# Performance work log

Hardware: AMD Instinct MI355X
Metric: run time of the kernel (lower is better)

Reference implementation:

```python
import jax, jax.numpy as jnp
import numpy as np

POSE_DIM = 16
H_DIM = 32
SEQ_LEN = 25
BATCH = 262144


def setup_inputs() -> dict:
    key = jax.random.key(0)
    ks = jax.random.split(key, 9)
    s = 0.1  # keep gates out of saturation
    return {
        "first_input": jax.random.normal(ks[0], (BATCH, POSE_DIM), dtype=jnp.float32),
        "h0": jax.random.normal(ks[1], (BATCH, H_DIM), dtype=jnp.float32),
        "c0": jax.random.normal(ks[2], (BATCH, H_DIM), dtype=jnp.float32),
        # LSTM params, torch layout/gate order (i, f, g, o)
        "W_ih": s * jax.random.normal(ks[3], (4 * H_DIM, POSE_DIM), dtype=jnp.float32),
        "W_hh": s * jax.random.normal(ks[4], (4 * H_DIM, H_DIM), dtype=jnp.float32),
        "b_ih": s * jax.random.normal(ks[5], (4 * H_DIM,), dtype=jnp.float32),
        "b_hh": s * jax.random.normal(ks[6], (4 * H_DIM,), dtype=jnp.float32),
        # hidden -> input-space projection
        "W_out": s * jax.random.normal(ks[7], (POSE_DIM, H_DIM), dtype=jnp.float32),
        "b_out": s * jax.random.normal(ks[8], (POSE_DIM,), dtype=jnp.float32),
    }


def reference(first_input, h0, c0, W_ih, W_hh, b_ih, b_hh, W_out, b_out):
    # Gate order matches torch.nn.LSTM: i, f, g, o.
    b = b_ih + b_hh  # [4H]

    def step(carry, _):
        x, h, c = carry  # x: [B, P], h/c: [B, H]
        gates = x @ W_ih.T + h @ W_hh.T + b  # [B, 4H]
        i, f, g, o = jnp.split(gates, 4, axis=-1)
        c = jax.nn.sigmoid(f) * c + jax.nn.sigmoid(i) * jnp.tanh(g)
        h = jax.nn.sigmoid(o) * jnp.tanh(c)
        x_next = h @ W_out.T + b_out  # projected back to pose space [B, P]
        return (x_next, h, c), x_next

    _, preds = jax.lax.scan(step, (first_input, h0, c0), None, length=SEQ_LEN)
    # preds: [S, B, P] -> [B, S, P] to match torch cat along dim=1
    return jnp.transpose(preds, (1, 0, 2))
```

## Files before the change

### kernel.cpp

```cpp
#include <hip/hip_runtime.h>
#include <hip/hip_bf16.h>


constexpr int P = 16;
constexpr int H = 32;
constexpr int S = 25;

typedef short        bf16x8 __attribute__((ext_vector_type(8)));
typedef float        f32x16 __attribute__((ext_vector_type(16)));
typedef float        f32x4  __attribute__((ext_vector_type(4)));
typedef unsigned int u32x4  __attribute__((ext_vector_type(4)));

union FragU { u32x4 u; bf16x8 b; };

#if __has_builtin(__builtin_amdgcn_exp2f)
#define EX2 __builtin_amdgcn_exp2f
#else
#define EX2 exp2f
#endif

__device__ __forceinline__ unsigned int pkbf(float lo, float hi) {
    unsigned short a = __builtin_bit_cast(unsigned short, __float2bfloat16(lo));
    unsigned short b = __builtin_bit_cast(unsigned short, __float2bfloat16(hi));
    return (unsigned int)a | ((unsigned int)b << 16);
}

__device__ __forceinline__ float gate_scale(int r) {
    return (r >= 64 && r < 96) ? -2.8853900817779268f
                               : -1.4426950408889634f;
}

__global__ void setup_frags(const float* __restrict__ Wih, const float* __restrict__ Whh,
                            const float* __restrict__ bih, const float* __restrict__ bhh,
                            const float* __restrict__ Wout, const float* __restrict__ bout,
                            unsigned int* __restrict__ ws)
{
    auto waug = [&](int r, int k) -> float {
        float s = (r < 128) ? gate_scale(r) : 1.0f;
        if (r < 128) {
            if (k < 32) {
                float a = Whh[r * H + k];
                for (int p = 0; p < P; ++p) a += Wih[r * P + p] * Wout[p * H + k];
                return s * a;
            }
            if (k == 32) {
                float a = bih[r] + bhh[r];
                for (int p = 0; p < P; ++p) a += Wih[r * P + p] * bout[p];
                return s * a;
            }
            return 0.0f;
        } else if (r < 144) {
            int p = r - 128;
            if (k < 32)  return Wout[p * H + k];
            if (k == 32) return bout[p];
            return 0.0f;
        }
        return 0.0f;
    };
    auto w0aug = [&](int r, int k) -> float {
        float s = gate_scale(r);
        if (k < 16)  return s * Wih[r * P + k];
        if (k < 48)  return s * Whh[r * H + (k - 16)];
        if (k == 48) return s * (bih[r] + bhh[r]);
        return 0.0f;
    };

    const int tid = threadIdx.x;
    for (int idx = tid; idx < 5 * 3 * 64 * 4; idx += 256) {
        int v = idx & 3, l = (idx >> 2) & 63, tc = idx >> 8;
        int t = tc / 3, c = tc % 3;
        int r = 32 * t + (l & 31);
        int k = 16 * c + 8 * (v >> 1) + 4 * (l >> 5) + 2 * (v & 1);
        ws[idx] = pkbf(waug(r, k), waug(r, k + 1));
    }
    for (int idx = tid; idx < 4 * 4 * 64 * 4; idx += 256) {
        int v = idx & 3, l = (idx >> 2) & 63, tc = idx >> 8;
        int t = tc / 4, c = tc % 4;
        int r = 32 * t + (l & 31);
        int k = 16 * c + 8 * (v >> 1) + 4 * (l >> 5) + 2 * (v & 1);
        ws[3840 + idx] = pkbf(w0aug(r, k), w0aug(r, k + 1));
    }
}

__global__ __launch_bounds__(256, 2) void decoder_mfma(
    const float* __restrict__ x0, const float* __restrict__ h0,
    const float* __restrict__ c0, const unsigned int* __restrict__ ws,
    float* __restrict__ out, int batch)
{
    const int lane = threadIdx.x & 63;
    const int wid  = threadIdx.x >> 6;
    const int bcol = lane & 31;
    const int hi   = lane >> 5;
    const int bg   = (blockIdx.x * 4 + wid) * 32 + bcol;
    if (bg >= batch) return;

    FragU A[5][3];
    #pragma unroll
    for (int t = 0; t < 5; ++t)
        #pragma unroll
        for (int c = 0; c < 3; ++c)
            A[t][c].u = *reinterpret_cast<const u32x4*>(ws + ((t * 3 + c) * 64 + lane) * 4);

    FragU Bbias;
    Bbias.u.x = (hi == 0) ? 0x3F80u : 0u;
    Bbias.u.y = 0u; Bbias.u.z = 0u; Bbias.u.w = 0u;

    float cc[16];
    #pragma unroll
    for (int q = 0; q < 4; ++q) {
        f32x4 t = *reinterpret_cast<const f32x4*>(c0 + (size_t)bg * H + q * 8 + 4 * hi);
        cc[q * 4 + 0] = t.x; cc[q * 4 + 1] = t.y; cc[q * 4 + 2] = t.z; cc[q * 4 + 3] = t.w;
    }

    const f32x16 vzero = {};
    f32x16 acc[4];

    {
        FragU B0[4];
        {
            const float* p = x0 + (size_t)bg * P;
            f32x4 a  = *reinterpret_cast<const f32x4*>(p + 4 * hi);
            f32x4 b4 = *reinterpret_cast<const f32x4*>(p + 8 + 4 * hi);
            B0[0].u.x = pkbf(a.x, a.y);  B0[0].u.y = pkbf(a.z, a.w);
            B0[0].u.z = pkbf(b4.x, b4.y); B0[0].u.w = pkbf(b4.z, b4.w);
        }
        #pragma unroll
        for (int ch = 0; ch < 2; ++ch) {
            const float* p = h0 + (size_t)bg * H + 16 * ch;
            f32x4 a  = *reinterpret_cast<const f32x4*>(p + 4 * hi);
            f32x4 b4 = *reinterpret_cast<const f32x4*>(p + 8 + 4 * hi);
            B0[1 + ch].u.x = pkbf(a.x, a.y);  B0[1 + ch].u.y = pkbf(a.z, a.w);
            B0[1 + ch].u.z = pkbf(b4.x, b4.y); B0[1 + ch].u.w = pkbf(b4.z, b4.w);
        }
        B0[3] = Bbias;

        #pragma unroll
        for (int t = 0; t < 4; ++t) acc[t] = vzero;
        #pragma unroll
        for (int c4 = 0; c4 < 4; ++c4) {
            #pragma unroll
            for (int t = 0; t < 4; ++t) {
                FragU a;
                a.u = *reinterpret_cast<const u32x4*>(ws + 3840 + ((t * 4 + c4) * 64 + lane) * 4);
                acc[t] = __builtin_amdgcn_mfma_f32_32x32x16_bf16(a.b, B0[c4].b, acc[t], 0, 0, 0);
            }
        }
    }

    FragU Bh[2];
    for (int s = 0; s < S; ++s) {
        float hh[16];
        #pragma unroll
        for (int r = 0; r < 16; ++r) {
            const float ei = EX2(acc[0][r]);
            const float ef = EX2(acc[1][r]);
            const float eg = EX2(acc[2][r]);
            const float eo = EX2(acc[3][r]);
            const float r1 = __builtin_amdgcn_rcpf((1.0f + ei) * (1.0f + eg));
            const float tg = (1.0f - eg) * r1;
            const float rf = __builtin_amdgcn_rcpf(1.0f + ef);
            const float cn = __builtin_fmaf(cc[r], rf, tg);
            cc[r] = cn;
            const float ec = EX2(cn * -2.8853900817779268f);
            const float r2 = __builtin_amdgcn_rcpf((1.0f + ec) * (1.0f + eo));
            hh[r] = (1.0f - ec) * r2;
        }

        Bh[0].u.x = pkbf(hh[0],  hh[1]);  Bh[0].u.y = pkbf(hh[2],  hh[3]);
        Bh[0].u.z = pkbf(hh[4],  hh[5]);  Bh[0].u.w = pkbf(hh[6],  hh[7]);
        Bh[1].u.x = pkbf(hh[8],  hh[9]);  Bh[1].u.y = pkbf(hh[10], hh[11]);
        Bh[1].u.z = pkbf(hh[12], hh[13]); Bh[1].u.w = pkbf(hh[14], hh[15]);

        f32x16 px;
        px = __builtin_amdgcn_mfma_f32_32x32x16_bf16(A[4][2].b, Bbias.b, vzero, 0, 0, 0);
        px = __builtin_amdgcn_mfma_f32_32x32x16_bf16(A[4][0].b, Bh[0].b, px,    0, 0, 0);
        px = __builtin_amdgcn_mfma_f32_32x32x16_bf16(A[4][1].b, Bh[1].b, px,    0, 0, 0);

        float* op = out + ((size_t)bg * S + s) * P + 4 * hi;
        f32x4 v0; v0.x = px[0]; v0.y = px[1]; v0.z = px[2]; v0.w = px[3];
        f32x4 v1; v1.x = px[4]; v1.y = px[5]; v1.z = px[6]; v1.w = px[7];
        __builtin_nontemporal_store(v0, reinterpret_cast<f32x4*>(op));
        __builtin_nontemporal_store(v1, reinterpret_cast<f32x4*>(op + 8));

        if (s + 1 < S) {
            #pragma unroll
            for (int t = 0; t < 4; ++t)
                acc[t] = __builtin_amdgcn_mfma_f32_32x32x16_bf16(A[t][2].b, Bbias.b, vzero, 0, 0, 0);
            #pragma unroll
            for (int ch = 0; ch < 2; ++ch)
                #pragma unroll
                for (int t = 0; t < 4; ++t)
                    acc[t] = __builtin_amdgcn_mfma_f32_32x32x16_bf16(A[t][ch].b, Bh[ch].b, acc[t], 0, 0, 0);
        }
    }
}

extern "C" void kernel_launch(void* const* d_in, const int* in_sizes, int n_in,
                              void* d_out, int out_size, void* d_ws, size_t ws_size,
                              hipStream_t stream) {
    const float* x0   = (const float*)d_in[0];
    const float* h0   = (const float*)d_in[1];
    const float* c0   = (const float*)d_in[2];
    const float* Wih  = (const float*)d_in[3];
    const float* Whh  = (const float*)d_in[4];
    const float* bih  = (const float*)d_in[5];
    const float* bhh  = (const float*)d_in[6];
    const float* Wout = (const float*)d_in[7];
    const float* bout = (const float*)d_in[8];
    float* out = (float*)d_out;
    unsigned int* ws = (unsigned int*)d_ws;

    const int batch = in_sizes[0] / P;

    hipLaunchKernelGGL(setup_frags, dim3(1), dim3(256), 0, stream,
                       Wih, Whh, bih, bhh, Wout, bout, ws);

    dim3 block(256);
    dim3 grid((batch + 127) / 128);
    hipLaunchKernelGGL(decoder_mfma, grid, block, 0, stream,
                       x0, h0, c0, ws, out, batch);
}
```

Before: 228.4 us.

## Process two independent batch tiles per wave to overlap MFMA and elementwise work

```diff
diff --git a/kernel.cpp b/kernel.cpp
--- a/kernel.cpp
+++ b/kernel.cpp
@@ -9,6 +9,7 @@
 typedef short        bf16x8 __attribute__((ext_vector_type(8)));
 typedef float        f32x16 __attribute__((ext_vector_type(16)));
 typedef float        f32x4  __attribute__((ext_vector_type(4)));
+typedef float        f32x2  __attribute__((ext_vector_type(2)));
 typedef unsigned int u32x4  __attribute__((ext_vector_type(4)));
 
 union FragU { u32x4 u; bf16x8 b; };
@@ -91,8 +92,10 @@
     const int wid  = threadIdx.x >> 6;
     const int bcol = lane & 31;
     const int hi   = lane >> 5;
-    const int bg   = (blockIdx.x * 4 + wid) * 32 + bcol;
-    if (bg >= batch) return;
+    const int base = (blockIdx.x * 4 + wid) * 64;
+    const int bg0  = base + bcol;
+    const int bg1  = base + 32 + bcol;
+    if (bg1 >= batch) return;
 
     FragU A[5][3];
     #pragma unroll
@@ -105,93 +108,126 @@
     Bbias.u.x = (hi == 0) ? 0x3F80u : 0u;
     Bbias.u.y = 0u; Bbias.u.z = 0u; Bbias.u.w = 0u;
 
-    float cc[16];
+    f32x2 cc0[8], cc1[8];
     #pragma unroll
     for (int q = 0; q < 4; ++q) {
-        f32x4 t = *reinterpret_cast<const f32x4*>(c0 + (size_t)bg * H + q * 8 + 4 * hi);
-        cc[q * 4 + 0] = t.x; cc[q * 4 + 1] = t.y; cc[q * 4 + 2] = t.z; cc[q * 4 + 3] = t.w;
+        f32x4 t0 = *reinterpret_cast<const f32x4*>(c0 + (size_t)bg0 * H + q * 8 + 4 * hi);
+        cc0[2 * q]     = f32x2{t0.x, t0.y};
+        cc0[2 * q + 1] = f32x2{t0.z, t0.w};
+        f32x4 t1 = *reinterpret_cast<const f32x4*>(c0 + (size_t)bg1 * H + q * 8 + 4 * hi);
+        cc1[2 * q]     = f32x2{t1.x, t1.y};
+        cc1[2 * q + 1] = f32x2{t1.z, t1.w};
     }
 
     const f32x16 vzero = {};
-    f32x16 acc[4];
+    f32x16 acc0[4], acc1[4];
+
+    auto EW = [&](f32x16 (&acc)[4], f32x2 (&cc)[8], f32x2 (&hh)[8]) {
+        const f32x2 one = {1.0f, 1.0f};
+        const f32x2 nk2 = {-2.8853900817779268f, -2.8853900817779268f};
+        #pragma unroll
+        for (int i = 0; i < 8; ++i) {
+            f32x2 Fi = {acc[0][2 * i], acc[0][2 * i + 1]};
+            f32x2 Ff = {acc[1][2 * i], acc[1][2 * i + 1]};
+            f32x2 Fg = {acc[2][2 * i], acc[2][2 * i + 1]};
+            f32x2 Fo = {acc[3][2 * i], acc[3][2 * i + 1]};
+            f32x2 ei, ef, eg, eo;
+            ei.x = EX2(Fi.x); ei.y = EX2(Fi.y);
+            ef.x = EX2(Ff.x); ef.y = EX2(Ff.y);
+            eg.x = EX2(Fg.x); eg.y = EX2(Fg.y);
+            eo.x = EX2(Fo.x); eo.y = EX2(Fo.y);
+            f32x2 d1 = (one + ei) * (one + eg);
+            f32x2 r1; r1.x = __builtin_amdgcn_rcpf(d1.x); r1.y = __builtin_amdgcn_rcpf(d1.y);
+            f32x2 tg = (one - eg) * r1;
+            f32x2 df = one + ef;
+            f32x2 rf; rf.x = __builtin_amdgcn_rcpf(df.x); rf.y = __builtin_amdgcn_rcpf(df.y);
+            f32x2 cn = cc[i] * rf + tg;
+            cc[i] = cn;
+            f32x2 ar = cn * nk2;
+            f32x2 ec; ec.x = EX2(ar.x); ec.y = EX2(ar.y);
+            f32x2 d2 = (one + ec) * (one + eo);
+            f32x2 r2; r2.x = __builtin_amdgcn_rcpf(d2.x); r2.y = __builtin_amdgcn_rcpf(d2.y);
+            hh[i] = (one - ec) * r2;
+        }
+    };
+    auto PACK = [&](f32x2 (&hh)[8], FragU (&Bh)[2]) {
+        Bh[0].u.x = pkbf(hh[0].x, hh[0].y); Bh[0].u.y = pkbf(hh[1].x, hh[1].y);
+        Bh[0].u.z = pkbf(hh[2].x, hh[2].y); Bh[0].u.w = pkbf(hh[3].x, hh[3].y);
+        Bh[1].u.x = pkbf(hh[4].x, hh[4].y); Bh[1].u.y = pkbf(hh[5].x, hh[5].y);
+        Bh[1].u.z = pkbf(hh[6].x, hh[6].y); Bh[1].u.w = pkbf(hh[7].x, hh[7].y);
+    };
+    auto PROJSTORE = [&](FragU (&Bh)[2], int bg, int s) {
+        f32x16 px;
+        px = __builtin_amdgcn_mfma_f32_32x32x16_bf16(A[4][2].b, Bbias.b, vzero, 0, 0, 0);
+        px = __builtin_amdgcn_mfma_f32_32x32x16_bf16(A[4][0].b, Bh[0].b, px,    0, 0, 0);
+        px = __builtin_amdgcn_mfma_f32_32x32x16_bf16(A[4][1].b, Bh[1].b, px,    0, 0, 0);
+        float* op = out + ((size_t)bg * S + s) * P + 4 * hi;
+        f32x4 v0 = {px[0], px[1], px[2], px[3]};
+        f32x4 v1 = {px[4], px[5], px[6], px[7]};
+        __builtin_nontemporal_store(v0, reinterpret_cast<f32x4*>(op));
+        __builtin_nontemporal_store(v1, reinterpret_cast<f32x4*>(op + 8));
+    };
+    auto GATES = [&](f32x16 (&acc)[4], FragU (&Bh)[2]) {
+        #pragma unroll
+        for (int t = 0; t < 4; ++t) {
+            f32x16 a;
+            a = __builtin_amdgcn_mfma_f32_32x32x16_bf16(A[t][2].b, Bbias.b, vzero, 0, 0, 0);
+            a = __builtin_amdgcn_mfma_f32_32x32x16_bf16(A[t][0].b, Bh[0].b, a,    0, 0, 0);
+            a = __builtin_amdgcn_mfma_f32_32x32x16_bf16(A[t][1].b, Bh[1].b, a,    0, 0, 0);
+            acc[t] = a;
+        }
+    };
 
     {
-        FragU B0[4];
+        FragU B00[4], B01[4];
         {
-            const float* p = x0 + (size_t)bg * P;
+            const float* p = x0 + (size_t)bg0 * P;
             f32x4 a  = *reinterpret_cast<const f32x4*>(p + 4 * hi);
             f32x4 b4 = *reinterpret_cast<const f32x4*>(p + 8 + 4 * hi);
-            B0[0].u.x = pkbf(a.x, a.y);  B0[0].u.y = pkbf(a.z, a.w);
-            B0[0].u.z = pkbf(b4.x, b4.y); B0[0].u.w = pkbf(b4.z, b4.w);
+            B00[0].u.x = pkbf(a.x, a.y);   B00[0].u.y = pkbf(a.z, a.w);
+            B00[0].u.z = pkbf(b4.x, b4.y); B00[0].u.w = pkbf(b4.z, b4.w);
+            p = x0 + (size_t)bg1 * P;
+            a  = *reinterpret_cast<const f32x4*>(p + 4 * hi);
+            b4 = *reinterpret_cast<const f32x4*>(p + 8 + 4 * hi);
+            B01[0].u.x = pkbf(a.x, a.y);   B01[0].u.y = pkbf(a.z, a.w);
+            B01[0].u.z = pkbf(b4.x, b4.y); B01[0].u.w = pkbf(b4.z, b4.w);
         }
         #pragma unroll
         for (int ch = 0; ch < 2; ++ch) {
-            const float* p = h0 + (size_t)bg * H + 16 * ch;
-            f32x4 a  = *reinterpret_cast<const f32x4*>(p + 4 * hi);
-            f32x4 b4 = *reinterpret_cast<const f32x4*>(p + 8 + 4 * hi);
-            B0[1 + ch].u.x = pkbf(a.x, a.y);  B0[1 + ch].u.y = pkbf(a.z, a.w);
-            B0[1 + ch].u.z = pkbf(b4.x, b4.y); B0[1 + ch].u.w = pkbf(b4.z, b4.w);
-        }
-        B0[3] = Bbias;
-
-        #pragma unroll
-        for (int t = 0; t < 4; ++t) acc[t] = vzero;
-        #pragma unroll
-        for (int c4 = 0; c4 < 4; ++c4) {
+            const float* q = h0 + (size_t)bg0 * H + 16 * ch;
+            f32x4 c4 = *reinterpret_cast<const f32x4*>(q + 4 * hi);
+            f32x4 d4 = *reinterpret_cast<const f32x4*>(q + 8 + 4 * hi);
+            B00[1 + ch].u.x = pkbf(c4.x, c4.y); B00[1 + ch].u.y = pkbf(c4.z, c4.w);
+            B00[1 + ch].u.z = pkbf(d4.x, d4.y); B00[1 + ch].u.w = pkbf(d4.z, d4.w);
+            q = h0 + (size_t)bg1 * H + 16 * ch;
+            c4 = *reinterpret_cast<const f32x4*>(q + 4 * hi);
+            d4 = *reinterpret_cast<const f32x4*>(q + 8 + 4 * hi);
+            B01[1 + ch].u.x = pkbf(c4.x, c4.y); B01[1 + ch].u.y = pkbf(c4.z, c4.w);
+            B01[1 + ch].u.z = pkbf(d4.x, d4.y); B01[1 + ch].u.w = pkbf(d4.z, d4.w);
+        }
+        B00[3] = Bbias; B01[3] = Bbias;
+        #pragma unroll
+        for (int t = 0; t < 4; ++t) { acc0[t] = vzero; acc1[t] = vzero; }
+        #pragma unroll
+        for (int c4 = 0; c4 < 4; ++c4)
             #pragma unroll
             for (int t = 0; t < 4; ++t) {
                 FragU a;
                 a.u = *reinterpret_cast<const u32x4*>(ws + 3840 + ((t * 4 + c4) * 64 + lane) * 4);
-                acc[t] = __builtin_amdgcn_mfma_f32_32x32x16_bf16(a.b, B0[c4].b, acc[t], 0, 0, 0);
+                acc0[t] = __builtin_amdgcn_mfma_f32_32x32x16_bf16(a.b, B00[c4].b, acc0[t], 0, 0, 0);
+                acc1[t] = __builtin_amdgcn_mfma_f32_32x32x16_bf16(a.b, B01[c4].b, acc1[t], 0, 0, 0);
             }
-        }
-    }
-
-    FragU Bh[2];
+    }
+
     for (int s = 0; s < S; ++s) {
-        float hh[16];
-        #pragma unroll
-        for (int r = 0; r < 16; ++r) {
-            const float ei = EX2(acc[0][r]);
-            const float ef = EX2(acc[1][r]);
-            const float eg = EX2(acc[2][r]);
-            const float eo = EX2(acc[3][r]);
-            const float r1 = __builtin_amdgcn_rcpf((1.0f + ei) * (1.0f + eg));
-            const float tg = (1.0f - eg) * r1;
-            const float rf = __builtin_amdgcn_rcpf(1.0f + ef);
-            const float cn = __builtin_fmaf(cc[r], rf, tg);
-            cc[r] = cn;
-            const float ec = EX2(cn * -2.8853900817779268f);
-            const float r2 = __builtin_amdgcn_rcpf((1.0f + ec) * (1.0f + eo));
-            hh[r] = (1.0f - ec) * r2;
-        }
-
-        Bh[0].u.x = pkbf(hh[0],  hh[1]);  Bh[0].u.y = pkbf(hh[2],  hh[3]);
-        Bh[0].u.z = pkbf(hh[4],  hh[5]);  Bh[0].u.w = pkbf(hh[6],  hh[7]);
-        Bh[1].u.x = pkbf(hh[8],  hh[9]);  Bh[1].u.y = pkbf(hh[10], hh[11]);
-        Bh[1].u.z = pkbf(hh[12], hh[13]); Bh[1].u.w = pkbf(hh[14], hh[15]);
-
-        f32x16 px;
-        px = __builtin_amdgcn_mfma_f32_32x32x16_bf16(A[4][2].b, Bbias.b, vzero, 0, 0, 0);
-        px = __builtin_amdgcn_mfma_f32_32x32x16_bf16(A[4][0].b, Bh[0].b, px,    0, 0, 0);
-        px = __builtin_amdgcn_mfma_f32_32x32x16_bf16(A[4][1].b, Bh[1].b, px,    0, 0, 0);
-
-        float* op = out + ((size_t)bg * S + s) * P + 4 * hi;
-        f32x4 v0; v0.x = px[0]; v0.y = px[1]; v0.z = px[2]; v0.w = px[3];
-        f32x4 v1; v1.x = px[4]; v1.y = px[5]; v1.z = px[6]; v1.w = px[7];
-        __builtin_nontemporal_store(v0, reinterpret_cast<f32x4*>(op));
-        __builtin_nontemporal_store(v1, reinterpret_cast<f32x4*>(op + 8));
-
-        if (s + 1 < S) {
-            #pragma unroll
-            for (int t = 0; t < 4; ++t)
-                acc[t] = __builtin_amdgcn_mfma_f32_32x32x16_bf16(A[t][2].b, Bbias.b, vzero, 0, 0, 0);
-            #pragma unroll
-            for (int ch = 0; ch < 2; ++ch)
-                #pragma unroll
-                for (int t = 0; t < 4; ++t)
-                    acc[t] = __builtin_amdgcn_mfma_f32_32x32x16_bf16(A[t][ch].b, Bh[ch].b, acc[t], 0, 0, 0);
-        }
+        f32x2 hh0[8]; FragU Bh0[2];
+        EW(acc0, cc0, hh0); PACK(hh0, Bh0);
+        PROJSTORE(Bh0, bg0, s);
+        if (s + 1 < S) GATES(acc0, Bh0);
+        f32x2 hh1[8]; FragU Bh1[2];
+        EW(acc1, cc1, hh1); PACK(hh1, Bh1);
+        PROJSTORE(Bh1, bg1, s);
+        if (s + 1 < S) GATES(acc1, Bh1);
     }
 }
 
@@ -216,7 +252,7 @@
                        Wih, Whh, bih, bhh, Wout, bout, ws);
 
     dim3 block(256);
-    dim3 grid((batch + 127) / 128);
+    dim3 grid((batch + 255) / 256);
     hipLaunchKernelGGL(decoder_mfma, grid, block, 0, stream,
                        x0, h0, c0, ws, out, batch);
 }
```

New measurement: 224.9 us. No clear change (-1.6%).

## Stage weight fragments in LDS and raise occupancy to four blocks per CU

Applied to the files above, without the earlier changes.

```diff
diff --git a/kernel.cpp b/kernel.cpp
--- a/kernel.cpp
+++ b/kernel.cpp
@@ -82,24 +82,29 @@
     }
 }
 
-__global__ __launch_bounds__(256, 2) void decoder_mfma(
+__global__ __launch_bounds__(256, 4) void decoder_mfma(
     const float* __restrict__ x0, const float* __restrict__ h0,
     const float* __restrict__ c0, const unsigned int* __restrict__ ws,
     float* __restrict__ out, int batch)
 {
+    __shared__ unsigned int Alds[5 * 3 * 64 * 4];
+
     const int lane = threadIdx.x & 63;
     const int wid  = threadIdx.x >> 6;
     const int bcol = lane & 31;
     const int hi   = lane >> 5;
     const int bg   = (blockIdx.x * 4 + wid) * 32 + bcol;
+
+    for (int i = threadIdx.x; i < 5 * 3 * 64 * 4; i += 256) Alds[i] = ws[i];
+    __syncthreads();
     if (bg >= batch) return;
 
-    FragU A[5][3];
-    #pragma unroll
-    for (int t = 0; t < 5; ++t)
-        #pragma unroll
-        for (int c = 0; c < 3; ++c)
-            A[t][c].u = *reinterpret_cast<const u32x4*>(ws + ((t * 3 + c) * 64 + lane) * 4);
+    const unsigned int* const Abase = Alds + lane * 4;
+    auto ldA = [&](int t, int c) -> FragU {
+        FragU a;
+        a.u = *reinterpret_cast<const u32x4*>(Abase + (t * 3 + c) * 256);
+        return a;
+    };
 
     FragU Bbias;
     Bbias.u.x = (hi == 0) ? 0x3F80u : 0u;
@@ -114,6 +119,7 @@
 
     const f32x16 vzero = {};
     f32x16 acc[4];
+    FragU Bh[2];
 
     {
         FragU B0[4];
@@ -147,51 +153,57 @@
         }
     }
 
-    FragU Bh[2];
-    for (int s = 0; s < S; ++s) {
-        float hh[16];
-        #pragma unroll
-        for (int r = 0; r < 16; ++r) {
-            const float ei = EX2(acc[0][r]);
-            const float ef = EX2(acc[1][r]);
-            const float eg = EX2(acc[2][r]);
-            const float eo = EX2(acc[3][r]);
-            const float r1 = __builtin_amdgcn_rcpf((1.0f + ei) * (1.0f + eg));
-            const float tg = (1.0f - eg) * r1;
-            const float rf = __builtin_amdgcn_rcpf(1.0f + ef);
-            const float cn = __builtin_fmaf(cc[r], rf, tg);
-            cc[r] = cn;
-            const float ec = EX2(cn * -2.8853900817779268f);
-            const float r2 = __builtin_amdgcn_rcpf((1.0f + ec) * (1.0f + eo));
-            hh[r] = (1.0f - ec) * r2;
-        }
-
-        Bh[0].u.x = pkbf(hh[0],  hh[1]);  Bh[0].u.y = pkbf(hh[2],  hh[3]);
-        Bh[0].u.z = pkbf(hh[4],  hh[5]);  Bh[0].u.w = pkbf(hh[6],  hh[7]);
-        Bh[1].u.x = pkbf(hh[8],  hh[9]);  Bh[1].u.y = pkbf(hh[10], hh[11]);
-        Bh[1].u.z = pkbf(hh[12], hh[13]); Bh[1].u.w = pkbf(hh[14], hh[15]);
-
+    auto EWPACK = [&]() {
+        #pragma unroll
+        for (int i = 0; i < 8; ++i) {
+            float h2[2];
+            #pragma unroll
+            for (int j = 0; j < 2; ++j) {
+                const int r = 2 * i + j;
+                const float ei = EX2(acc[0][r]);
+                const float ef = EX2(acc[1][r]);
+                const float eg = EX2(acc[2][r]);
+                const float eo = EX2(acc[3][r]);
+                const float r1 = __builtin_amdgcn_rcpf((1.0f + ei) * (1.0f + eg));
+                const float tg = (1.0f - eg) * r1;
+                const float rf = __builtin_amdgcn_rcpf(1.0f + ef);
+                const float cn = __builtin_fmaf(cc[r], rf, tg);
+                cc[r] = cn;
+                const float ec = EX2(cn * -2.8853900817779268f);
+                const float r2 = __builtin_amdgcn_rcpf((1.0f + ec) * (1.0f + eo));
+                h2[j] = (1.0f - ec) * r2;
+            }
+            Bh[i >> 2].u[i & 3] = pkbf(h2[0], h2[1]);
+        }
+    };
+    auto PROJSTORE = [&](int s) {
+        FragU a;
         f32x16 px;
-        px = __builtin_amdgcn_mfma_f32_32x32x16_bf16(A[4][2].b, Bbias.b, vzero, 0, 0, 0);
-        px = __builtin_amdgcn_mfma_f32_32x32x16_bf16(A[4][0].b, Bh[0].b, px,    0, 0, 0);
-        px = __builtin_amdgcn_mfma_f32_32x32x16_bf16(A[4][1].b, Bh[1].b, px,    0, 0, 0);
-
+        a = ldA(4, 2); px = __builtin_amdgcn_mfma_f32_32x32x16_bf16(a.b, Bbias.b, vzero, 0, 0, 0);
+        a = ldA(4, 0); px = __builtin_amdgcn_mfma_f32_32x32x16_bf16(a.b, Bh[0].b, px,    0, 0, 0);
+        a = ldA(4, 1); px = __builtin_amdgcn_mfma_f32_32x32x16_bf16(a.b, Bh[1].b, px,    0, 0, 0);
         float* op = out + ((size_t)bg * S + s) * P + 4 * hi;
-        f32x4 v0; v0.x = px[0]; v0.y = px[1]; v0.z = px[2]; v0.w = px[3];
-        f32x4 v1; v1.x = px[4]; v1.y = px[5]; v1.z = px[6]; v1.w = px[7];
+        f32x4 v0 = {px[0], px[1], px[2], px[3]};
+        f32x4 v1 = {px[4], px[5], px[6], px[7]};
         __builtin_nontemporal_store(v0, reinterpret_cast<f32x4*>(op));
         __builtin_nontemporal_store(v1, reinterpret_cast<f32x4*>(op + 8));
-
-        if (s + 1 < S) {
-            #pragma unroll
-            for (int t = 0; t < 4; ++t)
-                acc[t] = __builtin_amdgcn_mfma_f32_32x32x16_bf16(A[t][2].b, Bbias.b, vzero, 0, 0, 0);
-            #pragma unroll
-            for (int ch = 0; ch < 2; ++ch)
-                #pragma unroll
-                for (int t = 0; t < 4; ++t)
-                    acc[t] = __builtin_amdgcn_mfma_f32_32x32x16_bf16(A[t][ch].b, Bh[ch].b, acc[t], 0, 0, 0);
-        }
+    };
+    auto GATES = [&]() {
+        #pragma unroll
+        for (int t = 0; t < 4; ++t) {
+            FragU a;
+            f32x16 g;
+            a = ldA(t, 2); g = __builtin_amdgcn_mfma_f32_32x32x16_bf16(a.b, Bbias.b, vzero, 0, 0, 0);
+            a = ldA(t, 0); g = __builtin_amdgcn_mfma_f32_32x32x16_bf16(a.b, Bh[0].b, g,    0, 0, 0);
+            a = ldA(t, 1); g = __builtin_amdgcn_mfma_f32_32x32x16_bf16(a.b, Bh[1].b, g,    0, 0, 0);
+            acc[t] = g;
+        }
+    };
+
+    for (int s = 0; s < S; ++s) {
+        EWPACK();
+        PROJSTORE(s);
+        if (s + 1 < S) GATES();
     }
 }
 
```

New measurement: 233.9 us. 1.02x slower.
